# Optimization experiments

Hardware: AMD Instinct MI355X
Metric: run time of the kernel (lower is better)

Reference implementation:

```python
import jax, jax.numpy as jnp
import numpy as np

B, N, D = 4, 4096, 1024
H, DH = 16, 64            # heads, dim_head; inner = H*DH = 1024
FF = 4 * D                # ffn inner dim
EPS = 1e-5


def setup_inputs() -> dict:
    key = jax.random.key(0)
    ks = jax.random.split(key, 8)
    s = 0.02
    return {
        "x": jax.random.normal(ks[0], (B, N, D), jnp.float32),
        "W_qkv": jax.random.normal(ks[1], (D, 3 * H * DH), jnp.float32) * s,
        "W_out": jax.random.normal(ks[2], (H * DH, D), jnp.float32) * s,
        "b_out": jnp.zeros((D,), jnp.float32),
        "ln_g": jnp.ones((D,), jnp.float32),
        "ln_b": jnp.zeros((D,), jnp.float32),
        "W1": jax.random.normal(ks[3], (D, FF), jnp.float32) * s,
        "b1": jnp.zeros((FF,), jnp.float32),
        "W2": jax.random.normal(ks[4], (FF, D), jnp.float32) * s,
        "b2": jnp.zeros((D,), jnp.float32),
    }


def reference(x, W_qkv, W_out, b_out, ln_g, ln_b, W1, b1, W2, b2):
    b, n, _ = x.shape
    scale = DH ** -0.5

    # --- LinearAttention (dual-softmax kernelized attention) ---
    qkv = x @ W_qkv                                   # [b, n, 3*H*DH]
    q, k, v = jnp.split(qkv, 3, axis=-1)
    split = lambda t: t.reshape(b, n, H, DH).transpose(0, 2, 1, 3)  # [b, h, n, d]
    q = jax.nn.softmax(split(q) * scale, axis=-1)     # softmax over head dim
    k = jax.nn.softmax(split(k), axis=-2)             # softmax over sequence
    v = split(v)
    context = jnp.einsum('bhnd,bhne->bhde', q, k)     # [b, h, d, e] -- linear in n
    out = jnp.einsum('bhde,bhnd->bhne', context, v)   # [b, h, n, e]
    out = out.transpose(0, 2, 1, 3).reshape(b, n, H * DH)
    attn = out @ W_out + b_out                        # to_out (dropout=0 at eval)

    # --- LayerNorm ---
    mu = jnp.mean(attn, axis=-1, keepdims=True)
    var = jnp.var(attn, axis=-1, keepdims=True)
    h = (attn - mu) * jax.lax.rsqrt(var + EPS) * ln_g + ln_b

    # --- FeedForward: Linear -> SiLU -> Linear ---
    y = jax.nn.silu(h @ W1 + b1) @ W2 + b2
    return y
```

## Files before the change

### kernel.cpp

```cpp
#include <hip/hip_runtime.h>
#include <hip/hip_bf16.h>

typedef __bf16 bf16x8 __attribute__((ext_vector_type(8)));
typedef __bf16 bf16x4 __attribute__((ext_vector_type(4)));
typedef float  f32x4  __attribute__((ext_vector_type(4)));

#define GLOAD_LDS16(gp, lp) \
  __builtin_amdgcn_global_load_lds((const __attribute__((address_space(1))) void*)(gp), \
                                   (__attribute__((address_space(3))) void*)(lp), 16, 0, 0)


__global__ __launch_bounds__(256) void zero_f32(float* __restrict__ p, int n) {
  int i = (blockIdx.x * 256 + threadIdx.x) * 4;
  if (i < n) *(float4*)(p + i) = make_float4(0.f, 0.f, 0.f, 0.f);
}

__global__ __launch_bounds__(256) void cvt_f32_bf16(const float* __restrict__ in,
                                                    __bf16* __restrict__ out, long n) {
  long i = ((long)blockIdx.x * 256 + threadIdx.x) * 4;
  if (i >= n) return;
  float4 v = *(const float4*)(in + i);
  bf16x4 o;
  o[0] = (__bf16)v.x; o[1] = (__bf16)v.y; o[2] = (__bf16)v.z; o[3] = (__bf16)v.w;
  *(bf16x4*)(out + i) = o;
}

__global__ __launch_bounds__(256) void cvt_wT(const float* __restrict__ W,
                                              __bf16* __restrict__ WT, int K, int N) {
  __shared__ float t[32][33];
  int k0 = blockIdx.x * 32, n0 = blockIdx.y * 32;
  int tx = threadIdx.x, ty = threadIdx.y;
  #pragma unroll
  for (int i = 0; i < 32; i += 8)
    t[ty + i][tx] = W[(size_t)(k0 + ty + i) * N + n0 + tx];
  __syncthreads();
  #pragma unroll
  for (int i = 0; i < 32; i += 8)
    WT[(size_t)(n0 + ty + i) * K + k0 + tx] = (__bf16)t[tx][ty + i];
}


enum { EPI_BF16 = 0, EPI_F32_BIAS = 1, EPI_BF16_SILU = 2, EPI_BF16_BIAS = 3 };

template <int EPI>
__global__ __launch_bounds__(256, 2)
void gemm_bt(const __bf16* __restrict__ A, const __bf16* __restrict__ B,
             void* __restrict__ Cout, const float* __restrict__ bias,
             int M, int N, int K) {
  __shared__ __bf16 sA[128 * 32];
  __shared__ __bf16 sB[128 * 32];
  const int tid = threadIdx.x;
  const int w = tid >> 6, l = tid & 63;
  const int brow = blockIdx.x * 128;
  const int bcol = blockIdx.y * 128;
  const int wr = (w >> 1) * 64, wc = (w & 1) * 64;
  const int lr = l & 15, lk = (l >> 4) * 8;
  const int sr = l >> 2, sc = (l & 3) * 8;

  f32x4 acc[4][4] = {};

  for (int k0 = 0; k0 < K; k0 += 32) {
    #pragma unroll
    for (int ch = 0; ch < 2; ++ch) {
      int i = w * 2 + ch;
      int r = i * 16 + sr;
      GLOAD_LDS16(A + (size_t)(brow + r) * K + k0 + sc, sA + i * 512);
      GLOAD_LDS16(B + (size_t)(bcol + r) * K + k0 + sc, sB + i * 512);
    }
    __syncthreads();
    bf16x8 af[4], bf[4];
    #pragma unroll
    for (int m = 0; m < 4; ++m)
      af[m] = *(const bf16x8*)(sA + (wr + m * 16 + lr) * 32 + lk);
    #pragma unroll
    for (int n = 0; n < 4; ++n)
      bf[n] = *(const bf16x8*)(sB + (wc + n * 16 + lr) * 32 + lk);
    #pragma unroll
    for (int m = 0; m < 4; ++m)
      #pragma unroll
      for (int n = 0; n < 4; ++n)
        acc[m][n] = __builtin_amdgcn_mfma_f32_16x16x32_bf16(af[m], bf[n], acc[m][n], 0, 0, 0);
    __syncthreads();
  }

  #pragma unroll
  for (int m = 0; m < 4; ++m) {
    int row0 = brow + wr + m * 16 + (l >> 4) * 4;
    #pragma unroll
    for (int n = 0; n < 4; ++n) {
      int col = bcol + wc + n * 16 + lr;
      float bv = (EPI == EPI_BF16) ? 0.f : bias[col];
      #pragma unroll
      for (int j = 0; j < 4; ++j) {
        float v = acc[m][n][j];
        size_t off = (size_t)(row0 + j) * N + col;
        if (EPI == EPI_BF16) {
          ((__bf16*)Cout)[off] = (__bf16)v;
        } else if (EPI == EPI_F32_BIAS) {
          ((float*)Cout)[off] = v + bv;
        } else if (EPI == EPI_BF16_BIAS) {
          ((__bf16*)Cout)[off] = (__bf16)(v + bv);
        } else {
          float z = v + bv;
          ((__bf16*)Cout)[off] = (__bf16)(z / (1.f + __expf(-z)));
        }
      }
    }
  }
}


__global__ __launch_bounds__(256) void q_softmax(__bf16* __restrict__ qkv) {
  qkv += (size_t)blockIdx.z * 4096 * 3072;
  int wg = blockIdx.x * 4 + (threadIdx.x >> 6);
  int l = threadIdx.x & 63;
  int row = wg >> 4, h = wg & 15;
  __bf16* p = qkv + (size_t)row * 3072 + h * 64 + l;
  float v = (float)*p * 0.125f;
  float m = v;
  #pragma unroll
  for (int s = 32; s; s >>= 1) m = fmaxf(m, __shfl_xor(m, s));
  float e = __expf(v - m);
  float sum = e;
  #pragma unroll
  for (int s = 32; s; s >>= 1) sum += __shfl_xor(sum, s);
  *p = (__bf16)(e / sum);
}

__global__ __launch_bounds__(256) void k_exp(__bf16* __restrict__ qkv, float* __restrict__ S) {
  qkv += (size_t)blockIdx.z * 4096 * 3072;
  S   += (size_t)blockIdx.z * 1024;
  int c = blockIdx.x * 256 + threadIdx.x;
  int n0 = blockIdx.y * 128;
  float sum = 0.f;
  __bf16* base = qkv + (size_t)n0 * 3072 + 1024 + c;
  for (int i = 0; i < 128; ++i) {
    __bf16* p = base + (size_t)i * 3072;
    float e = __expf((float)*p);
    __bf16 eb = (__bf16)e;
    *p = eb;
    sum += (float)eb;
  }
  atomicAdd(&S[c], sum);
}

__global__ __launch_bounds__(256) void ctx_gemm(const __bf16* __restrict__ qkv,
                                                float* __restrict__ ctx) {
  qkv += (size_t)blockIdx.z * 4096 * 3072;
  ctx += (size_t)blockIdx.z * 16 * 4096;
  int h = blockIdx.x;
  int k0base = blockIdx.y * 1024;
  __shared__ __bf16 sQ[64 * 32];
  __shared__ __bf16 sK[64 * 32];
  int tid = threadIdx.x, w = tid >> 6, l = tid & 63;
  int lr = l & 15, lk = (l >> 4) * 8;
  int srow = tid >> 3, scol = (tid & 7) * 8;
  f32x4 acc[4] = {};

  for (int kc = 0; kc < 1024; kc += 32) {
    size_t grow = (size_t)(k0base + kc + srow) * 3072;
    bf16x8 qv = *(const bf16x8*)(qkv + grow + h * 64 + scol);
    bf16x8 kv = *(const bf16x8*)(qkv + grow + 1024 + h * 64 + scol);
    __syncthreads();
    #pragma unroll
    for (int j = 0; j < 8; ++j) {
      sQ[(scol + j) * 32 + srow] = qv[j];
      sK[(scol + j) * 32 + srow] = kv[j];
    }
    __syncthreads();
    bf16x8 a = *(const bf16x8*)(sQ + (w * 16 + lr) * 32 + lk);
    #pragma unroll
    for (int n = 0; n < 4; ++n) {
      bf16x8 bb = *(const bf16x8*)(sK + (n * 16 + lr) * 32 + lk);
      acc[n] = __builtin_amdgcn_mfma_f32_16x16x32_bf16(a, bb, acc[n], 0, 0, 0);
    }
  }
  float* cbase = ctx + (size_t)h * 64 * 64;
  #pragma unroll
  for (int n = 0; n < 4; ++n) {
    int col = n * 16 + lr;
    #pragma unroll
    for (int j = 0; j < 4; ++j) {
      int row = w * 16 + (l >> 4) * 4 + j;
      atomicAdd(cbase + row * 64 + col, acc[n][j]);
    }
  }
}

__global__ __launch_bounds__(256) void pv_gemm(const __bf16* __restrict__ qkv,
                                               const float* __restrict__ ctx,
                                               const float* __restrict__ S,
                                               __bf16* __restrict__ outpv) {
  qkv   += (size_t)blockIdx.z * 4096 * 3072;
  ctx   += (size_t)blockIdx.z * 16 * 4096;
  S     += (size_t)blockIdx.z * 1024;
  outpv += (size_t)blockIdx.z * 4096 * 1024;
  int h = blockIdx.y;
  int row0 = blockIdx.x * 128;
  __shared__ __bf16 sC[64 * 64];
  int tid = threadIdx.x;
  const float* cb = ctx + (size_t)h * 4096;
  for (int i = tid; i < 4096; i += 256) {
    int d = i >> 6, e = i & 63;
    sC[e * 64 + d] = (__bf16)cb[i];
  }
  __syncthreads();
  int w = tid >> 6, l = tid & 63;
  int lr = l & 15, lk = (l >> 4) * 8;
  f32x4 acc[2][4] = {};
  const __bf16* vbase = qkv + 2048 + h * 64;
  #pragma unroll
  for (int kk = 0; kk < 64; kk += 32) {
    #pragma unroll
    for (int m = 0; m < 2; ++m) {
      int r = row0 + w * 32 + m * 16 + lr;
      bf16x8 a = *(const bf16x8*)(vbase + (size_t)r * 3072 + kk + lk);
      #pragma unroll
      for (int n = 0; n < 4; ++n) {
        bf16x8 bb = *(const bf16x8*)(sC + (n * 16 + lr) * 64 + kk + lk);
        acc[m][n] = __builtin_amdgcn_mfma_f32_16x16x32_bf16(a, bb, acc[m][n], 0, 0, 0);
      }
    }
  }
  #pragma unroll
  for (int m = 0; m < 2; ++m) {
    int rb = row0 + w * 32 + m * 16 + (l >> 4) * 4;
    #pragma unroll
    for (int n = 0; n < 4; ++n) {
      int e = n * 16 + lr;
      float inv = 1.0f / S[h * 64 + e];
      #pragma unroll
      for (int j = 0; j < 4; ++j)
        outpv[(size_t)(rb + j) * 1024 + h * 64 + e] = (__bf16)(acc[m][n][j] * inv);
    }
  }
}

__global__ __launch_bounds__(256) void layernorm_k(const __bf16* __restrict__ attn,
                                                   const float* __restrict__ g,
                                                   const float* __restrict__ beta,
                                                   __bf16* __restrict__ out) {
  int row = blockIdx.x;
  int t = threadIdx.x;
  bf16x4 v4 = *(const bf16x4*)(attn + (size_t)row * 1024 + t * 4);
  float v0 = (float)v4[0], v1 = (float)v4[1], v2 = (float)v4[2], v3 = (float)v4[3];
  float s = v0 + v1 + v2 + v3;
  float ss = v0 * v0 + v1 * v1 + v2 * v2 + v3 * v3;
  #pragma unroll
  for (int sh = 32; sh; sh >>= 1) { s += __shfl_xor(s, sh); ss += __shfl_xor(ss, sh); }
  __shared__ float red[8];
  int w = t >> 6, l = t & 63;
  if (l == 0) { red[w] = s; red[4 + w] = ss; }
  __syncthreads();
  s = red[0] + red[1] + red[2] + red[3];
  ss = red[4] + red[5] + red[6] + red[7];
  float mu = s * (1.f / 1024.f);
  float var = ss * (1.f / 1024.f) - mu * mu;
  float rstd = rsqrtf(var + 1e-5f);
  float4 gg = *(const float4*)(g + t * 4);
  float4 bb = *(const float4*)(beta + t * 4);
  bf16x4 o;
  o[0] = (__bf16)((v0 - mu) * rstd * gg.x + bb.x);
  o[1] = (__bf16)((v1 - mu) * rstd * gg.y + bb.y);
  o[2] = (__bf16)((v2 - mu) * rstd * gg.z + bb.z);
  o[3] = (__bf16)((v3 - mu) * rstd * gg.w + bb.w);
  *(bf16x4*)(out + (size_t)row * 1024 + t * 4) = o;
}


extern "C" void kernel_launch(void* const* d_in, const int* in_sizes, int n_in,
                              void* d_out, int out_size, void* d_ws, size_t ws_size,
                              hipStream_t stream) {
  const float* x     = (const float*)d_in[0];
  const float* W_qkv = (const float*)d_in[1];
  const float* W_out = (const float*)d_in[2];
  const float* b_out = (const float*)d_in[3];
  const float* ln_g  = (const float*)d_in[4];
  const float* ln_b  = (const float*)d_in[5];
  const float* W1    = (const float*)d_in[6];
  const float* b1    = (const float*)d_in[7];
  const float* W2    = (const float*)d_in[8];
  const float* b2    = (const float*)d_in[9];

  char* ws = (char*)d_ws;
  size_t off = 0;
  auto alloc = [&](size_t bytes) { void* p = ws + off; off += (bytes + 255) & ~(size_t)255; return p; };

  __bf16* wqkvT = (__bf16*)alloc(3072ull * 1024 * 2);
  __bf16* woutT = (__bf16*)alloc(1024ull * 1024 * 2);
  __bf16* w1T   = (__bf16*)alloc(4096ull * 1024 * 2);
  __bf16* w2T   = (__bf16*)alloc(1024ull * 4096 * 2);

  cvt_wT<<<dim3(32, 96), dim3(32, 8), 0, stream>>>(W_qkv, wqkvT, 1024, 3072);
  cvt_wT<<<dim3(32, 32), dim3(32, 8), 0, stream>>>(W_out, woutT, 1024, 1024);
  cvt_wT<<<dim3(32, 128), dim3(32, 8), 0, stream>>>(W1, w1T, 1024, 4096);
  cvt_wT<<<dim3(128, 32), dim3(32, 8), 0, stream>>>(W2, w2T, 4096, 1024);

  const size_t FULL_NEED = 196ull << 20;

  if (ws_size >= FULL_NEED) {
    float*  Sctx  = (float*)alloc((4096ull + 4 * 16 * 4096) * 4);
    __bf16* xb    = (__bf16*)alloc(16384ull * 1024 * 2);
    __bf16* qkv   = (__bf16*)alloc(16384ull * 3072 * 2);
    __bf16* outpv = (__bf16*)alloc(16384ull * 1024 * 2);

    float* S   = Sctx;
    float* ctx = Sctx + 4096;
    __bf16* attn = (__bf16*)((char*)qkv + (64ull << 20));
    __bf16* hln  = xb;
    __bf16* ffn1 = qkv;

    cvt_f32_bf16<<<16384, 256, 0, stream>>>(x, xb, 16777216L);
    zero_f32<<<260, 256, 0, stream>>>(Sctx, 266240);

    gemm_bt<EPI_BF16><<<dim3(128, 24), 256, 0, stream>>>(xb, wqkvT, qkv, nullptr, 16384, 3072, 1024);
    q_softmax<<<dim3(16384, 1, 4), 256, 0, stream>>>(qkv);
    k_exp<<<dim3(4, 32, 4), 256, 0, stream>>>(qkv, S);
    ctx_gemm<<<dim3(16, 4, 4), 256, 0, stream>>>(qkv, ctx);
    pv_gemm<<<dim3(32, 16, 4), 256, 0, stream>>>(qkv, ctx, S, outpv);

    gemm_bt<EPI_BF16_BIAS><<<dim3(128, 8), 256, 0, stream>>>(outpv, woutT, attn, b_out, 16384, 1024, 1024);
    layernorm_k<<<16384, 256, 0, stream>>>(attn, ln_g, ln_b, hln);
    gemm_bt<EPI_BF16_SILU><<<dim3(128, 32), 256, 0, stream>>>(hln, w1T, ffn1, b1, 16384, 4096, 1024);
    gemm_bt<EPI_F32_BIAS><<<dim3(128, 8), 256, 0, stream>>>(ffn1, w2T, (float*)d_out, b2, 16384, 1024, 4096);
  } else {
    float*  Sctx  = (float*)alloc(66560ull * 4);
    __bf16* xb    = (__bf16*)alloc(16384ull * 1024 * 2);
    __bf16* outpv = (__bf16*)alloc(16384ull * 1024 * 2);
    __bf16* qkv_b = (__bf16*)alloc(4096ull * 3072 * 2);

    float* S   = Sctx;
    float* ctx = Sctx + 1024;
    __bf16* attn = xb;
    __bf16* hln  = outpv;
    __bf16* fchunk = xb;

    cvt_f32_bf16<<<16384, 256, 0, stream>>>(x, xb, 16777216L);

    for (int b = 0; b < 4; ++b) {
      const __bf16* xb_b = xb + (size_t)b * 4096 * 1024;
      gemm_bt<EPI_BF16><<<dim3(32, 24), 256, 0, stream>>>(xb_b, wqkvT, qkv_b, nullptr, 4096, 3072, 1024);
      zero_f32<<<65, 256, 0, stream>>>(Sctx, 66560);
      q_softmax<<<dim3(16384, 1, 1), 256, 0, stream>>>(qkv_b);
      k_exp<<<dim3(4, 32, 1), 256, 0, stream>>>(qkv_b, S);
      ctx_gemm<<<dim3(16, 4, 1), 256, 0, stream>>>(qkv_b, ctx);
      pv_gemm<<<dim3(32, 16, 1), 256, 0, stream>>>(qkv_b, ctx, S, outpv + (size_t)b * 4096 * 1024);
    }

    gemm_bt<EPI_BF16_BIAS><<<dim3(128, 8), 256, 0, stream>>>(outpv, woutT, attn, b_out, 16384, 1024, 1024);
    layernorm_k<<<16384, 256, 0, stream>>>(attn, ln_g, ln_b, hln);

    for (int c = 0; c < 4; ++c) {
      const __bf16* h_c = hln + (size_t)c * 4096 * 1024;
      float* out_c = (float*)d_out + (size_t)c * 4096 * 1024;
      gemm_bt<EPI_BF16_SILU><<<dim3(32, 32), 256, 0, stream>>>(h_c, w1T, fchunk, b1, 4096, 4096, 1024);
      gemm_bt<EPI_F32_BIAS><<<dim3(32, 8), 256, 0, stream>>>(fchunk, w2T, out_c, b2, 4096, 1024, 4096);
    }
  }
}
```

Measured before the change: 652.7 us.

## Replace GEMM with 256x256-tile, 4-stage pipelined, LDS-swizzled kernel

Replaces the 128x128 single-buffered GEMM with a 512-thread 256x256-tile kernel. It uses a 4-deep ring of LDS stages, filled by direct global-to-LDS loads and gated by explicit vmcnt waits. An XOR swizzle on LDS columns is meant to cut bank conflicts, and s_setprio around the MFMA bursts favours matrix issue. The larger tile raises data reuse per block and hides load latency, at the cost of 128KB LDS, one block per CU, and fewer blocks for wave balance.

```diff
diff --git a/kernel.cpp b/kernel.cpp
--- a/kernel.cpp
+++ b/kernel.cpp
@@ -4,6 +4,8 @@
 typedef __bf16 bf16x8 __attribute__((ext_vector_type(8)));
 typedef __bf16 bf16x4 __attribute__((ext_vector_type(4)));
 typedef float  f32x4  __attribute__((ext_vector_type(4)));
+
+#define SWZ 1
 
 #define GLOAD_LDS16(gp, lp) \
   __builtin_amdgcn_global_load_lds((const __attribute__((address_space(1))) void*)(gp), \
@@ -42,53 +44,95 @@
 
 enum { EPI_BF16 = 0, EPI_F32_BIAS = 1, EPI_BF16_SILU = 2, EPI_BF16_BIAS = 3 };
 
+__device__ __forceinline__ void stage_tile(const __bf16* __restrict__ A,
+                                           const __bf16* __restrict__ B,
+                                           __bf16* sAB,
+                                           int brow, int bcol, int K, int k0,
+                                           int w, int l) {
+  int rr = w * 16 + (l >> 2);
+  int oct = l & 3;
+#if SWZ
+  int c = (oct ^ (rr & 3)) * 8;
+#else
+  int c = oct * 8;
+#endif
+  GLOAD_LDS16(A + (size_t)(brow + rr) * K + k0 + c,       sAB + w * 512);
+  GLOAD_LDS16(A + (size_t)(brow + 128 + rr) * K + k0 + c, sAB + 4096 + w * 512);
+  GLOAD_LDS16(B + (size_t)(bcol + rr) * K + k0 + c,       sAB + 8192 + w * 512);
+  GLOAD_LDS16(B + (size_t)(bcol + 128 + rr) * K + k0 + c, sAB + 12288 + w * 512);
+}
+
 template <int EPI>
-__global__ __launch_bounds__(256, 2)
-void gemm_bt(const __bf16* __restrict__ A, const __bf16* __restrict__ B,
+__global__ __launch_bounds__(512, 1)
+void gemm256(const __bf16* __restrict__ A, const __bf16* __restrict__ B,
              void* __restrict__ Cout, const float* __restrict__ bias,
              int M, int N, int K) {
-  __shared__ __bf16 sA[128 * 32];
-  __shared__ __bf16 sB[128 * 32];
+  __shared__ __bf16 lds[4 * 16384];
   const int tid = threadIdx.x;
   const int w = tid >> 6, l = tid & 63;
-  const int brow = blockIdx.x * 128;
-  const int bcol = blockIdx.y * 128;
-  const int wr = (w >> 1) * 64, wc = (w & 1) * 64;
+  const int brow = blockIdx.x * 256;
+  const int bcol = blockIdx.y * 256;
+  const int wr = w >> 2, wc = w & 3;
   const int lr = l & 15, lk = (l >> 4) * 8;
-  const int sr = l >> 2, sc = (l & 3) * 8;
-
-  f32x4 acc[4][4] = {};
-
-  for (int k0 = 0; k0 < K; k0 += 32) {
-    #pragma unroll
-    for (int ch = 0; ch < 2; ++ch) {
-      int i = w * 2 + ch;
-      int r = i * 16 + sr;
-      GLOAD_LDS16(A + (size_t)(brow + r) * K + k0 + sc, sA + i * 512);
-      GLOAD_LDS16(B + (size_t)(bcol + r) * K + k0 + sc, sB + i * 512);
-    }
-    __syncthreads();
-    bf16x8 af[4], bf[4];
+#if SWZ
+  const int rdo = ((lk >> 3) ^ (lr & 3)) << 3;
+#else
+  const int rdo = lk;
+#endif
+  const int NT = K >> 5;
+
+  f32x4 acc[8][4] = {};
+
+  stage_tile(A, B, lds,           brow, bcol, K, 0,  w, l);
+  stage_tile(A, B, lds + 16384,   brow, bcol, K, 32, w, l);
+  stage_tile(A, B, lds + 32768,   brow, bcol, K, 64, w, l);
+
+  for (int t = 0; t < NT; ++t) {
+    if (t + 2 < NT)      asm volatile("s_waitcnt vmcnt(8)" ::: "memory");
+    else if (t + 1 < NT) asm volatile("s_waitcnt vmcnt(4)" ::: "memory");
+    else                 asm volatile("s_waitcnt vmcnt(0)" ::: "memory");
+    __builtin_amdgcn_s_barrier();
+    if (t + 3 < NT)
+      stage_tile(A, B, lds + ((t + 3) & 3) * 16384, brow, bcol, K, (t + 3) * 32, w, l);
+
+    const __bf16* sA = lds + (t & 3) * 16384;
+    const __bf16* sB = sA + 8192;
+
+    bf16x8 bfr[4], afr[4];
+    #pragma unroll
+    for (int n = 0; n < 4; ++n)
+      bfr[n] = *(const bf16x8*)(sB + (wc * 64 + n * 16 + lr) * 32 + rdo);
     #pragma unroll
     for (int m = 0; m < 4; ++m)
-      af[m] = *(const bf16x8*)(sA + (wr + m * 16 + lr) * 32 + lk);
-    #pragma unroll
-    for (int n = 0; n < 4; ++n)
-      bf[n] = *(const bf16x8*)(sB + (wc + n * 16 + lr) * 32 + lk);
+      afr[m] = *(const bf16x8*)(sA + (wr * 128 + m * 16 + lr) * 32 + rdo);
+
+    __builtin_amdgcn_s_setprio(1);
     #pragma unroll
     for (int m = 0; m < 4; ++m)
       #pragma unroll
       for (int n = 0; n < 4; ++n)
-        acc[m][n] = __builtin_amdgcn_mfma_f32_16x16x32_bf16(af[m], bf[n], acc[m][n], 0, 0, 0);
-    __syncthreads();
-  }
-
-  #pragma unroll
-  for (int m = 0; m < 4; ++m) {
-    int row0 = brow + wr + m * 16 + (l >> 4) * 4;
+        acc[m][n] = __builtin_amdgcn_mfma_f32_16x16x32_bf16(afr[m], bfr[n], acc[m][n], 0, 0, 0);
+    __builtin_amdgcn_s_setprio(0);
+
+    #pragma unroll
+    for (int m = 0; m < 4; ++m)
+      afr[m] = *(const bf16x8*)(sA + (wr * 128 + (m + 4) * 16 + lr) * 32 + rdo);
+
+    __builtin_amdgcn_s_setprio(1);
+    #pragma unroll
+    for (int m = 0; m < 4; ++m)
+      #pragma unroll
+      for (int n = 0; n < 4; ++n)
+        acc[m + 4][n] = __builtin_amdgcn_mfma_f32_16x16x32_bf16(afr[m], bfr[n], acc[m + 4][n], 0, 0, 0);
+    __builtin_amdgcn_s_setprio(0);
+  }
+
+  #pragma unroll
+  for (int m = 0; m < 8; ++m) {
+    int row0 = brow + wr * 128 + m * 16 + (l >> 4) * 4;
     #pragma unroll
     for (int n = 0; n < 4; ++n) {
-      int col = bcol + wc + n * 16 + lr;
+      int col = bcol + wc * 64 + n * 16 + lr;
       float bv = (EPI == EPI_BF16) ? 0.f : bias[col];
       #pragma unroll
       for (int j = 0; j < 4; ++j) {
@@ -313,16 +357,16 @@
     cvt_f32_bf16<<<16384, 256, 0, stream>>>(x, xb, 16777216L);
     zero_f32<<<260, 256, 0, stream>>>(Sctx, 266240);
 
-    gemm_bt<EPI_BF16><<<dim3(128, 24), 256, 0, stream>>>(xb, wqkvT, qkv, nullptr, 16384, 3072, 1024);
+    gemm256<EPI_BF16><<<dim3(64, 12), 512, 0, stream>>>(xb, wqkvT, qkv, nullptr, 16384, 3072, 1024);
     q_softmax<<<dim3(16384, 1, 4), 256, 0, stream>>>(qkv);
     k_exp<<<dim3(4, 32, 4), 256, 0, stream>>>(qkv, S);
     ctx_gemm<<<dim3(16, 4, 4), 256, 0, stream>>>(qkv, ctx);
     pv_gemm<<<dim3(32, 16, 4), 256, 0, stream>>>(qkv, ctx, S, outpv);
 
-    gemm_bt<EPI_BF16_BIAS><<<dim3(128, 8), 256, 0, stream>>>(outpv, woutT, attn, b_out, 16384, 1024, 1024);
+    gemm256<EPI_BF16_BIAS><<<dim3(64, 4), 512, 0, stream>>>(outpv, woutT, attn, b_out, 16384, 1024, 1024);
     layernorm_k<<<16384, 256, 0, stream>>>(attn, ln_g, ln_b, hln);
-    gemm_bt<EPI_BF16_SILU><<<dim3(128, 32), 256, 0, stream>>>(hln, w1T, ffn1, b1, 16384, 4096, 1024);
-    gemm_bt<EPI_F32_BIAS><<<dim3(128, 8), 256, 0, stream>>>(ffn1, w2T, (float*)d_out, b2, 16384, 1024, 4096);
+    gemm256<EPI_BF16_SILU><<<dim3(64, 16), 512, 0, stream>>>(hln, w1T, ffn1, b1, 16384, 4096, 1024);
+    gemm256<EPI_F32_BIAS><<<dim3(64, 4), 512, 0, stream>>>(ffn1, w2T, (float*)d_out, b2, 16384, 1024, 4096);
   } else {
     float*  Sctx  = (float*)alloc(66560ull * 4);
     __bf16* xb    = (__bf16*)alloc(16384ull * 1024 * 2);
@@ -339,7 +383,7 @@
 
     for (int b = 0; b < 4; ++b) {
       const __bf16* xb_b = xb + (size_t)b * 4096 * 1024;
-      gemm_bt<EPI_BF16><<<dim3(32, 24), 256, 0, stream>>>(xb_b, wqkvT, qkv_b, nullptr, 4096, 3072, 1024);
+      gemm256<EPI_BF16><<<dim3(16, 12), 512, 0, stream>>>(xb_b, wqkvT, qkv_b, nullptr, 4096, 3072, 1024);
       zero_f32<<<65, 256, 0, stream>>>(Sctx, 66560);
       q_softmax<<<dim3(16384, 1, 1), 256, 0, stream>>>(qkv_b);
       k_exp<<<dim3(4, 32, 1), 256, 0, stream>>>(qkv_b, S);
@@ -347,14 +391,14 @@
       pv_gemm<<<dim3(32, 16, 1), 256, 0, stream>>>(qkv_b, ctx, S, outpv + (size_t)b * 4096 * 1024);
     }
 
-    gemm_bt<EPI_BF16_BIAS><<<dim3(128, 8), 256, 0, stream>>>(outpv, woutT, attn, b_out, 16384, 1024, 1024);
+    gemm256<EPI_BF16_BIAS><<<dim3(64, 4), 512, 0, stream>>>(outpv, woutT, attn, b_out, 16384, 1024, 1024);
     layernorm_k<<<16384, 256, 0, stream>>>(attn, ln_g, ln_b, hln);
 
     for (int c = 0; c < 4; ++c) {
       const __bf16* h_c = hln + (size_t)c * 4096 * 1024;
       float* out_c = (float*)d_out + (size_t)c * 4096 * 1024;
-      gemm_bt<EPI_BF16_SILU><<<dim3(32, 32), 256, 0, stream>>>(h_c, w1T, fchunk, b1, 4096, 4096, 1024);
-      gemm_bt<EPI_F32_BIAS><<<dim3(32, 8), 256, 0, stream>>>(fchunk, w2T, out_c, b2, 4096, 1024, 4096);
-    }
-  }
-}
+      gemm256<EPI_BF16_SILU><<<dim3(16, 16), 512, 0, stream>>>(h_c, w1T, fchunk, b1, 4096, 4096, 1024);
+      gemm256<EPI_F32_BIAS><<<dim3(16, 4), 512, 0, stream>>>(fchunk, w2T, out_c, b2, 4096, 1024, 4096);
+    }
+  }
+}
```

Result: faster. 593.2 us (-9.1%).

## Double-buffer GEMM LDS tiles with async global-to-LDS prefetch and XOR swizzle

Applied to the files above, without the earlier changes.

Rewrites the bf16 GEMM main loop to use two LDS buffers, issuing global_load_lds for tile t+2 while MFMAs run on tile t, with manual vmcnt/lgkmcnt waits and barriers in place of the two __syncthreads per iteration. The K-octet index is XOR-swizzled by row so LDS fragment reads avoid bank conflicts, and s_setprio raises wave priority around the MFMA block. This targets load latency and LDS conflicts in all four large GEMMs, at the cost of doubled LDS per block (32 KB), which may limit occupancy, and fragile hand-written wait counts.

```diff
diff --git a/kernel.cpp b/kernel.cpp
--- a/kernel.cpp
+++ b/kernel.cpp
@@ -44,43 +44,73 @@
 
 template <int EPI>
 __global__ __launch_bounds__(256, 2)
-void gemm_bt(const __bf16* __restrict__ A, const __bf16* __restrict__ B,
+void gemm128(const __bf16* __restrict__ A, const __bf16* __restrict__ B,
              void* __restrict__ Cout, const float* __restrict__ bias,
              int M, int N, int K) {
-  __shared__ __bf16 sA[128 * 32];
-  __shared__ __bf16 sB[128 * 32];
+  __shared__ __bf16 lds[2 * 8192];
   const int tid = threadIdx.x;
   const int w = tid >> 6, l = tid & 63;
   const int brow = blockIdx.x * 128;
   const int bcol = blockIdx.y * 128;
   const int wr = (w >> 1) * 64, wc = (w & 1) * 64;
   const int lr = l & 15, lk = (l >> 4) * 8;
-  const int sr = l >> 2, sc = (l & 3) * 8;
+  const int rdo = ((lk >> 3) ^ ((lr >> 1) & 3)) << 3;
+  const int NT = K >> 5;
+
+  const int srow = w * 16 + (l >> 2);
+  const int oct = l & 3;
+  const int soct = oct ^ ((srow >> 1) & 3);
+  const __bf16* gA0 = A + (size_t)(brow + srow) * K + soct * 8;
+  const __bf16* gA1 = A + (size_t)(brow + 64 + srow) * K + soct * 8;
+  const __bf16* gB0 = B + (size_t)(bcol + srow) * K + soct * 8;
+  const __bf16* gB1 = B + (size_t)(bcol + 64 + srow) * K + soct * 8;
+  __bf16* const dA = lds + w * 512;
+  __bf16* const dB = lds + 4096 + w * 512;
 
   f32x4 acc[4][4] = {};
 
-  for (int k0 = 0; k0 < K; k0 += 32) {
-    #pragma unroll
-    for (int ch = 0; ch < 2; ++ch) {
-      int i = w * 2 + ch;
-      int r = i * 16 + sr;
-      GLOAD_LDS16(A + (size_t)(brow + r) * K + k0 + sc, sA + i * 512);
-      GLOAD_LDS16(B + (size_t)(bcol + r) * K + k0 + sc, sB + i * 512);
-    }
-    __syncthreads();
-    bf16x8 af[4], bf[4];
+  auto stage = [&](int buf) {
+    __bf16* a = dA + buf * 8192;
+    __bf16* b = dB + buf * 8192;
+    GLOAD_LDS16(gA0, a);
+    GLOAD_LDS16(gA1, a + 2048);
+    GLOAD_LDS16(gB0, b);
+    GLOAD_LDS16(gB1, b + 2048);
+    gA0 += 32; gA1 += 32; gB0 += 32; gB1 += 32;
+  };
+
+  stage(0); stage(1);
+
+  const int abase = (wr + lr) * 32 + rdo;
+  const int bbase = 4096 + (wc + lr) * 32 + rdo;
+
+  for (int t = 0; t < NT; ++t) {
+    if (t + 1 < NT) asm volatile("s_waitcnt vmcnt(4)" ::: "memory");
+    else            asm volatile("s_waitcnt vmcnt(0)" ::: "memory");
+    __builtin_amdgcn_s_barrier();
+
+    const __bf16* sA = lds + (t & 1) * 8192 + abase;
+    const __bf16* sB = lds + (t & 1) * 8192 + bbase;
+    bf16x8 afr[4], bfr[4];
     #pragma unroll
     for (int m = 0; m < 4; ++m)
-      af[m] = *(const bf16x8*)(sA + (wr + m * 16 + lr) * 32 + lk);
+      afr[m] = *(const bf16x8*)(sA + m * 512);
     #pragma unroll
     for (int n = 0; n < 4; ++n)
-      bf[n] = *(const bf16x8*)(sB + (wc + n * 16 + lr) * 32 + lk);
+      bfr[n] = *(const bf16x8*)(sB + n * 512);
+    asm volatile("s_waitcnt lgkmcnt(0)" ::: "memory");
+    __builtin_amdgcn_sched_barrier(0);
+    __builtin_amdgcn_s_barrier();
+
+    if (t + 2 < NT) stage(t & 1);
+
+    __builtin_amdgcn_s_setprio(1);
     #pragma unroll
     for (int m = 0; m < 4; ++m)
       #pragma unroll
       for (int n = 0; n < 4; ++n)
-        acc[m][n] = __builtin_amdgcn_mfma_f32_16x16x32_bf16(af[m], bf[n], acc[m][n], 0, 0, 0);
-    __syncthreads();
+        acc[m][n] = __builtin_amdgcn_mfma_f32_16x16x32_bf16(afr[m], bfr[n], acc[m][n], 0, 0, 0);
+    __builtin_amdgcn_s_setprio(0);
   }
 
   #pragma unroll
@@ -313,16 +343,16 @@
     cvt_f32_bf16<<<16384, 256, 0, stream>>>(x, xb, 16777216L);
     zero_f32<<<260, 256, 0, stream>>>(Sctx, 266240);
 
-    gemm_bt<EPI_BF16><<<dim3(128, 24), 256, 0, stream>>>(xb, wqkvT, qkv, nullptr, 16384, 3072, 1024);
+    gemm128<EPI_BF16><<<dim3(128, 24), 256, 0, stream>>>(xb, wqkvT, qkv, nullptr, 16384, 3072, 1024);
     q_softmax<<<dim3(16384, 1, 4), 256, 0, stream>>>(qkv);
     k_exp<<<dim3(4, 32, 4), 256, 0, stream>>>(qkv, S);
     ctx_gemm<<<dim3(16, 4, 4), 256, 0, stream>>>(qkv, ctx);
     pv_gemm<<<dim3(32, 16, 4), 256, 0, stream>>>(qkv, ctx, S, outpv);
 
-    gemm_bt<EPI_BF16_BIAS><<<dim3(128, 8), 256, 0, stream>>>(outpv, woutT, attn, b_out, 16384, 1024, 1024);
+    gemm128<EPI_BF16_BIAS><<<dim3(128, 8), 256, 0, stream>>>(outpv, woutT, attn, b_out, 16384, 1024, 1024);
     layernorm_k<<<16384, 256, 0, stream>>>(attn, ln_g, ln_b, hln);
-    gemm_bt<EPI_BF16_SILU><<<dim3(128, 32), 256, 0, stream>>>(hln, w1T, ffn1, b1, 16384, 4096, 1024);
-    gemm_bt<EPI_F32_BIAS><<<dim3(128, 8), 256, 0, stream>>>(ffn1, w2T, (float*)d_out, b2, 16384, 1024, 4096);
+    gemm128<EPI_BF16_SILU><<<dim3(128, 32), 256, 0, stream>>>(hln, w1T, ffn1, b1, 16384, 4096, 1024);
+    gemm128<EPI_F32_BIAS><<<dim3(128, 8), 256, 0, stream>>>(ffn1, w2T, (float*)d_out, b2, 16384, 1024, 4096);
   } else {
     float*  Sctx  = (float*)alloc(66560ull * 4);
     __bf16* xb    = (__bf16*)alloc(16384ull * 1024 * 2);
@@ -339,7 +369,7 @@
 
     for (int b = 0; b < 4; ++b) {
       const __bf16* xb_b = xb + (size_t)b * 4096 * 1024;
-      gemm_bt<EPI_BF16><<<dim3(32, 24), 256, 0, stream>>>(xb_b, wqkvT, qkv_b, nullptr, 4096, 3072, 1024);
+      gemm128<EPI_BF16><<<dim3(32, 24), 256, 0, stream>>>(xb_b, wqkvT, qkv_b, nullptr, 4096, 3072, 1024);
       zero_f32<<<65, 256, 0, stream>>>(Sctx, 66560);
       q_softmax<<<dim3(16384, 1, 1), 256, 0, stream>>>(qkv_b);
       k_exp<<<dim3(4, 32, 1), 256, 0, stream>>>(qkv_b, S);
@@ -347,14 +377,14 @@
       pv_gemm<<<dim3(32, 16, 1), 256, 0, stream>>>(qkv_b, ctx, S, outpv + (size_t)b * 4096 * 1024);
     }
 
-    gemm_bt<EPI_BF16_BIAS><<<dim3(128, 8), 256, 0, stream>>>(outpv, woutT, attn, b_out, 16384, 1024, 1024);
+    gemm128<EPI_BF16_BIAS><<<dim3(128, 8), 256, 0, stream>>>(outpv, woutT, attn, b_out, 16384, 1024, 1024);
     layernorm_k<<<16384, 256, 0, stream>>>(attn, ln_g, ln_b, hln);
 
     for (int c = 0; c < 4; ++c) {
       const __bf16* h_c = hln + (size_t)c * 4096 * 1024;
       float* out_c = (float*)d_out + (size_t)c * 4096 * 1024;
-      gemm_bt<EPI_BF16_SILU><<<dim3(32, 32), 256, 0, stream>>>(h_c, w1T, fchunk, b1, 4096, 4096, 1024);
-      gemm_bt<EPI_F32_BIAS><<<dim3(32, 8), 256, 0, stream>>>(fchunk, w2T, out_c, b2, 4096, 1024, 4096);
-    }
-  }
-}
+      gemm128<EPI_BF16_SILU><<<dim3(32, 32), 256, 0, stream>>>(h_c, w1T, fchunk, b1, 4096, 4096, 1024);
+      gemm128<EPI_F32_BIAS><<<dim3(32, 8), 256, 0, stream>>>(fchunk, w2T, out_c, b2, 4096, 1024, 4096);
+    }
+  }
+}
```

Result: no change. 656.4 us (+0.6%).
